# Kernel optimization log

Measured on AMD Instinct MI355X. Metric: run time of the kernel, lower is better.

The kernel has to match this reference:

```python
import jax, jax.numpy as jnp
import numpy as np

EMB = 1024
HEADS = 16
DK = EMB // HEADS

def setup_inputs() -> dict:
    key = jax.random.key(0)
    ks = jax.random.split(key, 5)
    scale = 0.02
    return {
        "x": jax.random.normal(ks[0], (4, 2048, EMB), dtype=jnp.float32),
        "W_in": jax.random.normal(ks[1], (3 * EMB, EMB), dtype=jnp.float32) * scale,
        "b_in": jax.random.normal(ks[2], (3 * EMB,), dtype=jnp.float32) * scale,
        "W_out": jax.random.normal(ks[3], (EMB, EMB), dtype=jnp.float32) * scale,
        "b_out": jax.random.normal(ks[4], (EMB,), dtype=jnp.float32) * scale,
    }

def reference(x, W_in, b_in, W_out, b_out):
    B, T, C = x.shape
    qkv = x @ W_in.T + b_in                      # [B,T,3C]
    q, k, v = jnp.split(qkv, 3, axis=-1)
    def heads(t):
        return t.reshape(B, T, HEADS, DK).transpose(0, 2, 1, 3)  # [B,H,T,Dk]
    q, k, v = heads(q), heads(k), heads(v)
    scores = jnp.einsum("bhqd,bhkd->bhqk", q, k) / jnp.sqrt(jnp.float32(DK))
    causal = jnp.tril(jnp.ones((T, T), dtype=bool))
    scores = jnp.where(causal, scores, jnp.finfo(scores.dtype).min)
    attn = jax.nn.softmax(scores, axis=-1)
    y = jnp.einsum("bhqk,bhkd->bhqd", attn, v)   # [B,H,T,Dk]
    y = y.transpose(0, 2, 1, 3).reshape(B, T, C)
    return y @ W_out.T + b_out
```

## Files before the change

### kernel.cpp

```cpp
#include <hip/hip_runtime.h>
#include <hip/hip_bf16.h>

#define EMB   1024
#define HEADS 16
#define DKV   64
#define BB    4
#define TT    2048
#define MTOT  8192

#define QSCALE 0.1803368801111204f

typedef short bf16x8 __attribute__((ext_vector_type(8)));
typedef float f32x4  __attribute__((ext_vector_type(4)));

__device__ __forceinline__ ushort bf16_bits(float f) {
    union { __hip_bfloat16 h; ushort u; } cv;
    cv.h = __float2bfloat16(f);
    return cv.u;
}
__device__ __forceinline__ unsigned pack_bf16(float lo, float hi) {
    return (unsigned)bf16_bits(lo) | ((unsigned)bf16_bits(hi) << 16);
}
__device__ __forceinline__ void gload16(const void* g, void* lds) {
    __builtin_amdgcn_global_load_lds(
        (const __attribute__((address_space(1))) unsigned*)g,
        (__attribute__((address_space(3))) unsigned*)lds, 16, 0, 0);
}
__device__ __forceinline__ int swz128(int row, int bytecol) {
    return row * 128 + (bytecol ^ ((row & 7) << 4));
}

__global__ void cvt_all(const float* __restrict__ x,   ushort* __restrict__ xo,
                        const float* __restrict__ wi,  ushort* __restrict__ wio,
                        const float* __restrict__ wo,  ushort* __restrict__ woo) {
    const int n4x = (MTOT * EMB) / 4;
    const int n4i = (3 * EMB * EMB) / 4;
    const int n4o = (EMB * EMB) / 4;
    int idx = blockIdx.x * blockDim.x + threadIdx.x;
    int stride = gridDim.x * blockDim.x;
    for (int i = idx; i < n4x + n4i + n4o; i += stride) {
        const float* in;
        ushort* out;
        int j = i;
        if (j < n4x)            { in = x;  out = xo;  }
        else if (j < n4x + n4i) { in = wi; out = wio; j -= n4x; }
        else                    { in = wo; out = woo; j -= n4x + n4i; }
        float4 v = reinterpret_cast<const float4*>(in)[j];
        ushort4 o;
        o.x = bf16_bits(v.x);
        o.y = bf16_bits(v.y);
        o.z = bf16_bits(v.z);
        o.w = bf16_bits(v.w);
        reinterpret_cast<ushort4*>(out)[j] = o;
    }
}

template<int EPI>
__global__ __launch_bounds__(256) void gemm_bt(
    const ushort* __restrict__ Ab, const ushort* __restrict__ Wb,
    const float* __restrict__ bias,
    ushort* __restrict__ qo, ushort* __restrict__ ko, ushort* __restrict__ vo,
    float* __restrict__ outf,
    int Msz, int Nsz, int Ksz)
{
    __shared__ __align__(16) ushort Sh[6][128 * 32];

    int tid = threadIdx.x;
    int mtiles = Msz >> 7;
    int bm = blockIdx.x % mtiles;
    int bn = blockIdx.x / mtiles;
    int m0 = bm << 7, n0 = bn << 7;
    int w = tid >> 6, l = tid & 63;
    int wr = w >> 1, wc = w & 1;
    int lr = l & 15, lk = (l >> 4) << 3;
    int srow = w * 16 + (l >> 2);
    int scol = (l & 3) << 3;

    f32x4 acc[4][4] = {};

    auto STAGE = [&](int buf, int k0) {
        #pragma unroll
        for (int p = 0; p < 2; ++p) {
            int row = p * 64 + srow;
            gload16(&Ab[(size_t)(m0 + row) * Ksz + k0 + scol],
                    (char*)Sh[buf * 2]     + (size_t)(p * 256 + w * 64) * 16);
            gload16(&Wb[(size_t)(n0 + row) * Ksz + k0 + scol],
                    (char*)Sh[buf * 2 + 1] + (size_t)(p * 256 + w * 64) * 16);
        }
    };

    const int nk = Ksz >> 5;
    STAGE(0, 0);
    STAGE(1, 32);
    int buf = 0, sbuf = 2;
    for (int t = 0; t < nk; ++t) {
        if (t + 1 < nk) asm volatile("s_waitcnt vmcnt(4)" ::: "memory");
        else            asm volatile("s_waitcnt vmcnt(0)" ::: "memory");
        __builtin_amdgcn_s_barrier();
        __builtin_amdgcn_sched_barrier(0);

        const ushort* As = Sh[buf * 2];
        const ushort* Bs = Sh[buf * 2 + 1];
        bf16x8 a[4], b[4];
        #pragma unroll
        for (int mi = 0; mi < 4; ++mi)
            a[mi] = *(const bf16x8*)(&As[(wr * 64 + mi * 16 + lr) * 32 + lk]);
        #pragma unroll
        for (int ni = 0; ni < 4; ++ni)
            b[ni] = *(const bf16x8*)(&Bs[(wc * 64 + ni * 16 + lr) * 32 + lk]);

        if (t + 2 < nk) STAGE(sbuf, (t + 2) << 5);

        __builtin_amdgcn_s_setprio(1);
        #pragma unroll
        for (int mi = 0; mi < 4; ++mi)
            #pragma unroll
            for (int ni = 0; ni < 4; ++ni)
                acc[mi][ni] = __builtin_amdgcn_mfma_f32_16x16x32_bf16(
                    a[mi], b[ni], acc[mi][ni], 0, 0, 0);
        __builtin_amdgcn_s_setprio(0);

        buf = (buf == 2) ? 0 : buf + 1;
        sbuf = (sbuf == 2) ? 0 : sbuf + 1;
    }

    if (EPI == 1) {
        #pragma unroll
        for (int mi = 0; mi < 4; ++mi)
            #pragma unroll
            for (int ni = 0; ni < 4; ++ni) {
                int n = n0 + wc * 64 + ni * 16 + lr;
                float bv = bias[n];
                #pragma unroll
                for (int r = 0; r < 4; ++r) {
                    int m = m0 + wr * 64 + mi * 16 + ((l >> 4) << 2) + r;
                    outf[(size_t)m * Nsz + n] = acc[mi][ni][r] + bv;
                }
            }
    } else {
        int which = n0 >> 10;
        if (which < 2) {
            ushort* dst = (which == 0) ? qo : ko;
            float qs = (which == 0) ? QSCALE : 1.f;
            #pragma unroll
            for (int mi = 0; mi < 4; ++mi)
                #pragma unroll
                for (int ni = 0; ni < 4; ++ni) {
                    int n = n0 + wc * 64 + ni * 16 + lr;
                    float bv = bias[n];
                    int rem = n & 1023;
                    int hd = rem >> 6, dk = rem & 63;
                    #pragma unroll
                    for (int r = 0; r < 4; ++r) {
                        int m = m0 + wr * 64 + mi * 16 + ((l >> 4) << 2) + r;
                        int b_ = m >> 11, t_ = m & 2047;
                        dst[((((size_t)b_ * HEADS + hd) * TT + t_) << 6) + dk] =
                            bf16_bits((acc[mi][ni][r] + bv) * qs);
                    }
                }
        } else {
            char* Tb = (char*)Sh;
            int b_ = m0 >> 11;
            int row_r = tid >> 1;
            int rem = (n0 + row_r) & 1023;
            int hd = rem >> 6, dk = rem & 63;
            size_t vrow = ((size_t)(b_ * HEADS + hd) * DKV + dk) * TT;
            int tbase = (m0 & 2047) + (tid & 1) * 32;
            #pragma unroll
            for (int h = 0; h < 2; ++h) {
                __syncthreads();
                if (wr == h) {
                    #pragma unroll
                    for (int ni = 0; ni < 4; ++ni) {
                        int n_l = wc * 64 + ni * 16 + lr;
                        float bv = bias[n0 + n_l];
                        #pragma unroll
                        for (int mi = 0; mi < 4; ++mi) {
                            uint2 u;
                            u.x = pack_bf16(acc[mi][ni][0] + bv, acc[mi][ni][1] + bv);
                            u.y = pack_bf16(acc[mi][ni][2] + bv, acc[mi][ni][3] + bv);
                            *(uint2*)(Tb + swz128(n_l, mi * 32 + ((l >> 4) << 3))) = u;
                        }
                    }
                }
                __syncthreads();
                #pragma unroll
                for (int qq = 0; qq < 4; ++qq) {
                    int4 d = *(const int4*)(Tb + swz128(row_r, (tid & 1) * 64 + qq * 16));
                    *(int4*)(&vo[vrow + tbase + h * 64 + qq * 8]) = d;
                }
            }
        }
    }
}

__device__ __forceinline__ void strip_tile(
    const char* __restrict__ Kbuf, const char* __restrict__ Vbuf, char* __restrict__ Plw,
    bf16x8 q0, bf16x8 q1,
    float& l_run, f32x4 (&o)[4],
    int lr, int g, bool diag, int qloc)
{
    f32x4 st[4];
    #pragma unroll
    for (int kt = 0; kt < 4; ++kt) {
        bf16x8 a0 = *(const bf16x8*)(Kbuf + swz128(kt * 16 + lr, g * 16));
        bf16x8 a1 = *(const bf16x8*)(Kbuf + swz128(kt * 16 + lr, 64 + g * 16));
        f32x4 z = {};
        __builtin_amdgcn_s_setprio(1);
        z = __builtin_amdgcn_mfma_f32_16x16x32_bf16(a0, q0, z, 0, 0, 0);
        z = __builtin_amdgcn_mfma_f32_16x16x32_bf16(a1, q1, z, 0, 0, 0);
        __builtin_amdgcn_s_setprio(0);
        st[kt] = z;
    }
    if (diag) {
        #pragma unroll
        for (int kt = 0; kt < 4; ++kt)
            #pragma unroll
            for (int r = 0; r < 4; ++r) {
                int kvloc = kt * 16 + g * 4 + r;
                st[kt][r] = (kvloc <= qloc) ? st[kt][r] : -1e30f;
            }
    }

    float rs = 0.f;
    #pragma unroll
    for (int kt = 0; kt < 4; ++kt) {
        float p0 = exp2f(st[kt][0]);
        float p1 = exp2f(st[kt][1]);
        float p2 = exp2f(st[kt][2]);
        float p3 = exp2f(st[kt][3]);
        rs += (p0 + p1) + (p2 + p3);
        uint2 u;
        u.x = pack_bf16(p0, p1);
        u.y = pack_bf16(p2, p3);
        *(uint2*)(Plw + swz128(lr, kt * 32 + g * 8)) = u;
    }
    rs += __shfl_xor(rs, 16);
    rs += __shfl_xor(rs, 32);
    l_run += rs;

    bf16x8 pa0 = *(const bf16x8*)(Plw + swz128(lr, g * 16));
    bf16x8 pa1 = *(const bf16x8*)(Plw + swz128(lr, 64 + g * 16));

    __builtin_amdgcn_s_setprio(1);
    #pragma unroll
    for (int dt = 0; dt < 4; ++dt) {
        bf16x8 b0 = *(const bf16x8*)(Vbuf + swz128(dt * 16 + lr, g * 16));
        bf16x8 b1 = *(const bf16x8*)(Vbuf + swz128(dt * 16 + lr, 64 + g * 16));
        o[dt] = __builtin_amdgcn_mfma_f32_16x16x32_bf16(pa0, b0, o[dt], 0, 0, 0);
        o[dt] = __builtin_amdgcn_mfma_f32_16x16x32_bf16(pa1, b1, o[dt], 0, 0, 0);
    }
    __builtin_amdgcn_s_setprio(0);
}

__global__ __launch_bounds__(256, 3) void attn_kernel(
    const ushort* __restrict__ qb, const ushort* __restrict__ kb,
    const ushort* __restrict__ vtb, ushort* __restrict__ yb)
{
    __shared__ __align__(16) char Ks[2][64 * 128];
    __shared__ __align__(16) char Vs[2][64 * 128];
    __shared__ __align__(16) char Pl[4][16 * 128];

    int tid = threadIdx.x;
    int w = tid >> 6, l = tid & 63;
    int bid = blockIdx.x;
    int swz = (bid & 7) * 128 + (bid >> 3);
    int pair = swz & 15;
    int bh = swz >> 4;
    int qtA = 31 - pair, qtB = pair;

    const ushort* Q  = qb  + (size_t)bh * TT * DKV;
    const ushort* K  = kb  + (size_t)bh * TT * DKV;
    const ushort* Vt = vtb + (size_t)bh * DKV * TT;
    int lr = l & 15, g = l >> 4;
    int qA0 = qtA * 64 + w * 16;
    int qB0 = qtB * 64 + w * 16;

    bf16x8 qaA0 = *(const bf16x8*)(&Q[(size_t)(qA0 + lr) * DKV + g * 8]);
    bf16x8 qaA1 = *(const bf16x8*)(&Q[(size_t)(qA0 + lr) * DKV + 32 + g * 8]);
    bf16x8 qaB0 = *(const bf16x8*)(&Q[(size_t)(qB0 + lr) * DKV + g * 8]);
    bf16x8 qaB1 = *(const bf16x8*)(&Q[(size_t)(qB0 + lr) * DKV + 32 + g * 8]);

    int srow = w * 8 + (l >> 3);
    int scel = ((((l & 7) * 16) ^ ((l >> 3) << 4)) >> 1);

    float lA = 0.f, lB = 0.f;
    f32x4 oA[4] = {}, oB[4] = {};
    int nt = qtA + 1;

    #pragma unroll
    for (int p = 0; p < 2; ++p) {
        int row = p * 32 + srow;
        gload16(&K [(size_t)row * DKV + scel], (char*)Ks[0] + (size_t)(p * 256 + w * 64) * 16);
        gload16(&Vt[(size_t)row * TT  + scel], (char*)Vs[0] + (size_t)(p * 256 + w * 64) * 16);
    }

    for (int jt = 0; jt < nt; ++jt) {
        int buf = jt & 1;
        __syncthreads();

        if (jt + 1 < nt) {
            int kv1 = (jt + 1) * 64;
            #pragma unroll
            for (int p = 0; p < 2; ++p) {
                int row = p * 32 + srow;
                gload16(&K [(size_t)(kv1 + row) * DKV + scel],
                        (char*)Ks[buf ^ 1] + (size_t)(p * 256 + w * 64) * 16);
                gload16(&Vt[(size_t)row * TT + kv1 + scel],
                        (char*)Vs[buf ^ 1] + (size_t)(p * 256 + w * 64) * 16);
            }
        }

        strip_tile(Ks[buf], Vs[buf], Pl[w], qaA0, qaA1, lA, oA,
                   lr, g, jt == qtA, w * 16 + lr);
        if (jt <= qtB)
            strip_tile(Ks[buf], Vs[buf], Pl[w], qaB0, qaB1, lB, oB,
                       lr, g, jt == qtB, w * 16 + lr);
    }

    int b_ = bh >> 4, h_ = bh & 15;
    {
        float li0 = 1.f / __shfl(lA, g * 4 + 0);
        float li1 = 1.f / __shfl(lA, g * 4 + 1);
        float li2 = 1.f / __shfl(lA, g * 4 + 2);
        float li3 = 1.f / __shfl(lA, g * 4 + 3);
        #pragma unroll
        for (int dt = 0; dt < 4; ++dt) {
            int d_ = h_ * 64 + dt * 16 + lr;
            size_t base = ((size_t)b_ * TT + (qA0 + g * 4)) * EMB + d_;
            yb[base]           = bf16_bits(oA[dt][0] * li0);
            yb[base + EMB]     = bf16_bits(oA[dt][1] * li1);
            yb[base + 2 * EMB] = bf16_bits(oA[dt][2] * li2);
            yb[base + 3 * EMB] = bf16_bits(oA[dt][3] * li3);
        }
    }
    {
        float li0 = 1.f / __shfl(lB, g * 4 + 0);
        float li1 = 1.f / __shfl(lB, g * 4 + 1);
        float li2 = 1.f / __shfl(lB, g * 4 + 2);
        float li3 = 1.f / __shfl(lB, g * 4 + 3);
        #pragma unroll
        for (int dt = 0; dt < 4; ++dt) {
            int d_ = h_ * 64 + dt * 16 + lr;
            size_t base = ((size_t)b_ * TT + (qB0 + g * 4)) * EMB + d_;
            yb[base]           = bf16_bits(oB[dt][0] * li0);
            yb[base + EMB]     = bf16_bits(oB[dt][1] * li1);
            yb[base + 2 * EMB] = bf16_bits(oB[dt][2] * li2);
            yb[base + 3 * EMB] = bf16_bits(oB[dt][3] * li3);
        }
    }
}

extern "C" void kernel_launch(void* const* d_in, const int* in_sizes, int n_in,
                              void* d_out, int out_size, void* d_ws, size_t ws_size,
                              hipStream_t stream) {
    const float* x     = (const float*)d_in[0];
    const float* W_in  = (const float*)d_in[1];
    const float* b_in  = (const float*)d_in[2];
    const float* W_out = (const float*)d_in[3];
    const float* b_out = (const float*)d_in[4];
    float* out = (float*)d_out;
    char* ws = (char*)d_ws;

    ushort* xb  = (ushort*)(ws);
    ushort* wib = (ushort*)(ws + 16777216);
    ushort* wob = (ushort*)(ws + 23068672);
    ushort* qbp = (ushort*)(ws + 25165824);
    ushort* kbp = (ushort*)(ws + 41943040);
    ushort* vbp = (ushort*)(ws + 58720256);
    ushort* ybp = (ushort*)(ws + 75497472);

    cvt_all<<<1280, 256, 0, stream>>>(x, xb, W_in, wib, W_out, wob);

    gemm_bt<0><<<dim3((MTOT / 128) * (3 * EMB / 128)), dim3(256), 0, stream>>>(
        xb, wib, b_in, qbp, kbp, vbp, nullptr, MTOT, 3 * EMB, EMB);

    attn_kernel<<<dim3(BB * HEADS * 16), dim3(256), 0, stream>>>(
        qbp, kbp, vbp, ybp);

    gemm_bt<1><<<dim3((MTOT / 128) * (EMB / 128)), dim3(256), 0, stream>>>(
        ybp, wob, b_out, nullptr, nullptr, nullptr, out, MTOT, EMB, EMB);
}
```

Baseline: 173.4 us.

## Load V operands directly from global into registers, defer row-sum reduction

Removes the LDS staging buffers for V. Each wave now loads its V^T MFMA operands straight from global memory into registers at the start of every KV tile, and both strip calls reuse them. The cross-lane row-sum shuffles move out of the inner loop and run once after it, which works because the sum is linear. This cuts LDS traffic and footprint, which may allow higher occupancy, but adds redundant uncached-latency global loads per wave with no prefetch. Those loads may stall the MFMA pipeline.

```diff
diff --git a/kernel.cpp b/kernel.cpp
--- a/kernel.cpp
+++ b/kernel.cpp
@@ -195,7 +195,9 @@
 }
 
 __device__ __forceinline__ void strip_tile(
-    const char* __restrict__ Kbuf, const char* __restrict__ Vbuf, char* __restrict__ Plw,
+    const char* __restrict__ Kbuf,
+    const bf16x8 (&vb0)[4], const bf16x8 (&vb1)[4],
+    char* __restrict__ Plw,
     bf16x8 q0, bf16x8 q1,
     float& l_run, f32x4 (&o)[4],
     int lr, int g, bool diag, int qloc)
@@ -235,8 +237,6 @@
         u.y = pack_bf16(p2, p3);
         *(uint2*)(Plw + swz128(lr, kt * 32 + g * 8)) = u;
     }
-    rs += __shfl_xor(rs, 16);
-    rs += __shfl_xor(rs, 32);
     l_run += rs;
 
     bf16x8 pa0 = *(const bf16x8*)(Plw + swz128(lr, g * 16));
@@ -245,10 +245,8 @@
     __builtin_amdgcn_s_setprio(1);
     #pragma unroll
     for (int dt = 0; dt < 4; ++dt) {
-        bf16x8 b0 = *(const bf16x8*)(Vbuf + swz128(dt * 16 + lr, g * 16));
-        bf16x8 b1 = *(const bf16x8*)(Vbuf + swz128(dt * 16 + lr, 64 + g * 16));
-        o[dt] = __builtin_amdgcn_mfma_f32_16x16x32_bf16(pa0, b0, o[dt], 0, 0, 0);
-        o[dt] = __builtin_amdgcn_mfma_f32_16x16x32_bf16(pa1, b1, o[dt], 0, 0, 0);
+        o[dt] = __builtin_amdgcn_mfma_f32_16x16x32_bf16(pa0, vb0[dt], o[dt], 0, 0, 0);
+        o[dt] = __builtin_amdgcn_mfma_f32_16x16x32_bf16(pa1, vb1[dt], o[dt], 0, 0, 0);
     }
     __builtin_amdgcn_s_setprio(0);
 }
@@ -258,7 +256,6 @@
     const ushort* __restrict__ vtb, ushort* __restrict__ yb)
 {
     __shared__ __align__(16) char Ks[2][64 * 128];
-    __shared__ __align__(16) char Vs[2][64 * 128];
     __shared__ __align__(16) char Pl[4][16 * 128];
 
     int tid = threadIdx.x;
@@ -291,32 +288,43 @@
     #pragma unroll
     for (int p = 0; p < 2; ++p) {
         int row = p * 32 + srow;
-        gload16(&K [(size_t)row * DKV + scel], (char*)Ks[0] + (size_t)(p * 256 + w * 64) * 16);
-        gload16(&Vt[(size_t)row * TT  + scel], (char*)Vs[0] + (size_t)(p * 256 + w * 64) * 16);
+        gload16(&K[(size_t)row * DKV + scel], (char*)Ks[0] + (size_t)(p * 256 + w * 64) * 16);
     }
 
     for (int jt = 0; jt < nt; ++jt) {
         int buf = jt & 1;
+        int kv0 = jt * 64;
         __syncthreads();
 
+        bf16x8 vb0[4], vb1[4];
+        #pragma unroll
+        for (int dt = 0; dt < 4; ++dt) {
+            const ushort* Vrow = Vt + (size_t)(dt * 16 + lr) * TT + kv0 + g * 8;
+            vb0[dt] = *(const bf16x8*)(Vrow);
+            vb1[dt] = *(const bf16x8*)(Vrow + 32);
+        }
+
         if (jt + 1 < nt) {
-            int kv1 = (jt + 1) * 64;
+            int kv1 = kv0 + 64;
             #pragma unroll
             for (int p = 0; p < 2; ++p) {
                 int row = p * 32 + srow;
-                gload16(&K [(size_t)(kv1 + row) * DKV + scel],
+                gload16(&K[(size_t)(kv1 + row) * DKV + scel],
                         (char*)Ks[buf ^ 1] + (size_t)(p * 256 + w * 64) * 16);
-                gload16(&Vt[(size_t)row * TT + kv1 + scel],
-                        (char*)Vs[buf ^ 1] + (size_t)(p * 256 + w * 64) * 16);
             }
         }
 
-        strip_tile(Ks[buf], Vs[buf], Pl[w], qaA0, qaA1, lA, oA,
+        strip_tile(Ks[buf], vb0, vb1, Pl[w], qaA0, qaA1, lA, oA,
                    lr, g, jt == qtA, w * 16 + lr);
         if (jt <= qtB)
-            strip_tile(Ks[buf], Vs[buf], Pl[w], qaB0, qaB1, lB, oB,
+            strip_tile(Ks[buf], vb0, vb1, Pl[w], qaB0, qaB1, lB, oB,
                        lr, g, jt == qtB, w * 16 + lr);
     }
+
+    lA += __shfl_xor(lA, 16);
+    lA += __shfl_xor(lA, 32);
+    lB += __shfl_xor(lB, 16);
+    lB += __shfl_xor(lB, 32);
 
     int b_ = bh >> 4, h_ = bh & 15;
     {
```

Result: slower. 246.8 us (+42.3%).
